# Kernel optimization log

Hardware: AMD Instinct MI355X
Metric: run time of the kernel (lower is better)

## Reference

```python
import jax, jax.numpy as jnp
import numpy as np

B, N, DIM, H, DH = 2, 2048, 512, 8, 64
INNER = H * DH  # == DIM, required by the q.view trick in the original module
STEP = 4


def setup_inputs() -> dict:
    key = jax.random.key(0)
    k1, k2, k3 = jax.random.split(key, 3)
    x = jax.random.normal(k1, (B, N, DIM), jnp.float32)
    # to_qkv: Linear(dim, 4*inner_dim, bias=False); stored as [in, out] for x @ W
    W_qkv = jax.random.normal(k2, (DIM, 4 * INNER), jnp.float32) * 0.02
    # to_out: Linear(2*inner_dim, dim) with bias
    W_out = jax.random.normal(k3, (2 * INNER, DIM), jnp.float32) * 0.02
    b_out = jnp.zeros((DIM,), jnp.float32)
    return {"x": x, "W_qkv": W_qkv, "W_out": W_out, "b_out": b_out}


def reference(x, W_qkv, W_out, b_out):
    b, n, _ = x.shape
    h, dh = H, DH
    scale = dh ** -0.5

    qkvt = x @ W_qkv                       # [b, n, 4*inner]
    q, k, v, t = jnp.split(qkvt, 4, axis=-1)
    to_heads = lambda z: z.reshape(b, n, h, dh).transpose(0, 2, 1, 3)  # [b,h,n,dh]
    q, k, v, t = map(to_heads, (q, k, v, t))

    # pad q by repeating its last row yushu times (note: yushu=4 when n%4==0)
    yushu = STEP - n % STEP
    q = jnp.concatenate([q, jnp.repeat(q[:, :, -1:, :], yushu, axis=2)], axis=2)
    q0 = q.reshape(b, h, STEP, (n + yushu) // STEP, dh)[:, :, 0]  # [b,h,(n+yushu)/4,dh]
    q = jnp.tile(q0, (1, 1, STEP, 1))[:, :, :n]                   # [b,h,n,dh]

    dots = jnp.einsum('bhnd,bhmd->bhnm', q, k) * scale
    attn1 = jax.nn.softmax(dots, axis=-1)

    # fixed distance-decay attention: exp(-|i-j|/e), column-normalized
    pos = jnp.arange(1, n + 1, dtype=x.dtype)
    tg = jnp.abs(pos[None, :] - pos[:, None])                     # [n, n]
    attn2 = jnp.exp(-tg / jnp.exp(jnp.asarray(1.0, x.dtype)))
    # torch: attn2 / attn2.sum(-1) broadcasts [n] over last axis (divides column j by row-sum j)
    attn2 = attn2 / attn2.sum(-1)

    out1 = jnp.einsum('bhnm,bhmd->bhnd', attn1, v)
    out2 = jnp.einsum('nm,bhmd->bhnd', attn2, t)  # attn2 shared across b,h; no repeat needed
    out = jnp.concatenate([out1, out2], axis=-1)   # [b,h,n,2*dh]
    out = out.transpose(0, 2, 1, 3).reshape(b, n, 2 * h * dh)  # b n (h d)
    return out @ W_out + b_out  # dropout=0.0 -> identity
```

## Files before the change

### kernel.cpp

```cpp
#include <hip/hip_runtime.h>

#define NSEQ 2048
#define NB   2
#define NH   8

typedef unsigned short u16;
typedef __attribute__((ext_vector_type(8))) short s8v;
typedef __attribute__((ext_vector_type(4))) float f4v;

static __device__ __forceinline__ u16 f2bf(float f) {
  unsigned u = __float_as_uint(f);
  unsigned r = (u + 0x7fffu + ((u >> 16) & 1u)) >> 16;
  return (u16)r;
}
static __device__ __forceinline__ u16 f2bf_fast(float f) {
  return (u16)((__float_as_uint(f) + 0x8000u) >> 16);
}
static __device__ __forceinline__ unsigned pk2(float a, float b) {
  return (unsigned)f2bf(a) | ((unsigned)f2bf(b) << 16);
}
static __device__ __forceinline__ float bf2f(u16 v) {
  return __uint_as_float(((unsigned)v) << 16);
}

typedef __attribute__((address_space(3))) unsigned int lds_u32;
typedef const __attribute__((address_space(1))) unsigned int glob_u32;
static __device__ __forceinline__ void load16(const void* g, void* l) {
  __builtin_amdgcn_global_load_lds((glob_u32*)g, (lds_u32*)l, 16, 0, 0);
}

__global__ __launch_bounds__(256)
void prep_kernel(const float* __restrict__ x, const float* __restrict__ Wqkv,
                 const float* __restrict__ Wout, u16* __restrict__ xb,
                 u16* __restrict__ WqkvT, u16* __restrict__ Wc) {
  __shared__ float tile[32][33];
  const int bid = blockIdx.x;
  if (bid < 1024) {
    long i = ((long)bid * 256 + threadIdx.x) * 8;
    float4 a = *(const float4*)&x[i];
    float4 b = *(const float4*)&x[i + 4];
    uint4 w;
    w.x = pk2(a.x, a.y); w.y = pk2(a.z, a.w);
    w.z = pk2(b.x, b.y); w.w = pk2(b.z, b.w);
    *(uint4*)&xb[i] = w;
    return;
  }
  const int tx = threadIdx.x & 31, ty = threadIdx.x >> 5;
  if (bid < 2048) {
    int b2 = bid - 1024;
    int c0 = (b2 & 63) * 32, r0 = (b2 >> 6) * 32;
#pragma unroll
    for (int s = 0; s < 32; s += 8)
      tile[ty + s][tx] = Wqkv[(long)(r0 + ty + s) * 2048 + c0 + tx];
    __syncthreads();
#pragma unroll
    for (int s = 0; s < 32; s += 8)
      WqkvT[(long)(c0 + ty + s) * 512 + r0 + tx] = f2bf(tile[tx][ty + s]);
    return;
  }
  {
    int b3 = bid - 2048;
    int part = b3 >= 256;
    if (part) b3 -= 256;
    int c0 = (b3 & 15) * 32, r0 = (b3 >> 4) * 32;
#pragma unroll
    for (int s = 0; s < 32; s += 8) {
      int k = r0 + ty + s;
      int srcrow = ((k >> 6) * 128) + part * 64 + (k & 63);
      tile[ty + s][tx] = Wout[(long)srcrow * 512 + c0 + tx];
    }
    __syncthreads();
    int koff = part ? 0 : 512;
#pragma unroll
    for (int s = 0; s < 32; s += 8) {
      long o = (long)(c0 + ty + s) * 1024 + koff + r0 + tx;
      Wc[o] = f2bf(tile[tx][ty + s]);
    }
  }
}

__global__ __launch_bounds__(256)
void gemm1_fused(const u16* __restrict__ xb, const u16* __restrict__ WqkvT,
                 u16* __restrict__ qkvtb, u16* __restrict__ qu,
                 u16* __restrict__ VtG) {
  const int bid = blockIdx.x;
  const bool isq = bid >= 768;
  int bxk, by;
  if (!isq) { bxk = bid % 24; by = bid / 24; }
  else { int b2 = bid - 768; bxk = b2 & 7; by = b2 >> 3; }
  __shared__ alignas(16) u16 As[128 * 64];
  __shared__ alignas(16) u16 Bs[64 * 64];
  const int tid = threadIdx.x, lane = tid & 63, wave = tid >> 6;
  const int l15 = lane & 15, quad = lane >> 4;
  const int wr = wave >> 1, wc = wave & 1;
  const int Brow0 = isq ? bxk * 64 : 512 + bxk * 64;

  int offA[4], offB[2];
  long baseA[4], baseB[2];
#pragma unroll
  for (int c = 0; c < 4; ++c) {
    int off = (c * 4 + wave) * 1024 + lane * 16;
    int r = off >> 7;
    int cp = (off & 127) >> 4;
    int cb = ((cp ^ (r & 7)) << 3);
    offA[c] = off;
    int gar;
    if (!isq) {
      gar = by * 128 + r;
    } else {
      int rr = by * 128 + r;
      int b = rr >= 576;
      int s = rr - (b ? 576 : 0);
      if (s >= 513) s -= 513;
      gar = b * 2048 + s;
    }
    baseA[c] = (long)gar * 512 + cb;
  }
#pragma unroll
  for (int c = 0; c < 2; ++c) {
    int off = (c * 4 + wave) * 1024 + lane * 16;
    int r = off >> 7, cp = (off & 127) >> 4;
    int cb = ((cp ^ (r & 7)) << 3);
    offB[c] = off;
    baseB[c] = (long)(Brow0 + r) * 512 + cb;
  }

  f4v acc[4][2];
#pragma unroll
  for (int i = 0; i < 4; ++i)
#pragma unroll
    for (int j = 0; j < 2; ++j) acc[i][j] = (f4v){0.f, 0.f, 0.f, 0.f};

  for (int k0 = 0; k0 < 512; k0 += 64) {
    __syncthreads();
#pragma unroll
    for (int c = 0; c < 4; ++c)
      load16(&xb[baseA[c] + k0], ((char*)As) + offA[c]);
#pragma unroll
    for (int c = 0; c < 2; ++c)
      load16(&WqkvT[baseB[c] + k0], ((char*)Bs) + offB[c]);
    __syncthreads();

#pragma unroll
    for (int ksub = 0; ksub < 2; ++ksub) {
      const int cc = (((ksub << 2) | quad) ^ (l15 & 7)) << 3;
      s8v bf[2];
#pragma unroll
      for (int j = 0; j < 2; ++j)
        bf[j] = *(const s8v*)&Bs[(wc * 32 + j * 16 + l15) * 64 + cc];
#pragma unroll
      for (int i = 0; i < 4; ++i) {
        s8v af = *(const s8v*)&As[(wr * 64 + i * 16 + l15) * 64 + cc];
#pragma unroll
        for (int j = 0; j < 2; ++j)
          acc[i][j] = __builtin_amdgcn_mfma_f32_16x16x32_bf16(af, bf[j], acc[i][j], 0, 0, 0);
      }
    }
  }

  const bool isv = (!isq) && bxk >= 8 && bxk < 16;
#pragma unroll
  for (int i = 0; i < 4; ++i) {
    int row0 = by * 128 + wr * 64 + i * 16 + quad * 4;
    if (isv) {
      int b = row0 >> 11, n = row0 & 2047;
#pragma unroll
      for (int j = 0; j < 2; ++j) {
        int vcol = (bxk - 8) * 64 + wc * 32 + j * 16 + l15;
        int h = vcol >> 6, d = vcol & 63;
        uint2 w;
        w.x = pk2(acc[i][j][0], acc[i][j][1]);
        w.y = pk2(acc[i][j][2], acc[i][j][3]);
        *(uint2*)&VtG[(((long)b * 8 + h) * 64 + d) * 2048 + n] = w;
      }
    } else {
#pragma unroll
      for (int rr = 0; rr < 4; ++rr) {
        int row = row0 + rr;
#pragma unroll
        for (int j = 0; j < 2; ++j) {
          int col = wc * 32 + j * 16 + l15;
          u16 v = f2bf(acc[i][j][rr]);
          if (!isq)
            qkvtb[(long)row * 2048 + 512 + bxk * 64 + col] = v;
          else
            qu[(long)row * 512 + bxk * 64 + col] = v;
        }
      }
    }
  }
}

__global__ __launch_bounds__(256)
void gemm2_merged(const u16* __restrict__ O2, const u16* __restrict__ O1u,
                  const u16* __restrict__ Wc, const float* __restrict__ bias,
                  float* __restrict__ C) {
  __shared__ alignas(16) u16 As[64 * 64];
  __shared__ alignas(16) u16 Bs[64 * 64];
  const int tid = threadIdx.x, lane = tid & 63, wave = tid >> 6;
  const int l15 = lane & 15, quad = lane >> 4;
  const int wr = wave >> 1, wc = wave & 1;
  const long m0 = (long)blockIdx.y * 64, n0 = (long)blockIdx.x * 64;

  int offA[2], offB[2];
  long baseO2[2], baseO1[2], baseB[2];
#pragma unroll
  for (int c = 0; c < 2; ++c) {
    int off = (c * 4 + wave) * 1024 + lane * 16;
    int r = off >> 7, cp = (off & 127) >> 4;
    int cb = ((cp ^ (r & 7)) << 3);
    offA[c] = off; offB[c] = off;
    long rowA = m0 + r;
    int b = (int)(rowA >> 11);
    int eff = (int)(rowA & 2047) % 513;
    baseO2[c] = rowA * 512 + cb;
    baseO1[c] = ((long)(b * 576 + eff)) * 512 + cb;
    baseB[c] = (long)(n0 + r) * 1024 + cb;
  }

  f4v acc[2][2];
#pragma unroll
  for (int i = 0; i < 2; ++i)
#pragma unroll
    for (int j = 0; j < 2; ++j) acc[i][j] = (f4v){0.f, 0.f, 0.f, 0.f};

  for (int k0 = 0; k0 < 1024; k0 += 64) {
    __syncthreads();
#pragma unroll
    for (int c = 0; c < 2; ++c) {
      const u16* src = (k0 < 512) ? &O2[baseO2[c] + k0] : &O1u[baseO1[c] + k0 - 512];
      load16(src, ((char*)As) + offA[c]);
      load16(&Wc[baseB[c] + k0], ((char*)Bs) + offB[c]);
    }
    __syncthreads();

#pragma unroll
    for (int ksub = 0; ksub < 2; ++ksub) {
      const int cc = (((ksub << 2) | quad) ^ (l15 & 7)) << 3;
      s8v bf[2];
#pragma unroll
      for (int j = 0; j < 2; ++j)
        bf[j] = *(const s8v*)&Bs[(wc * 32 + j * 16 + l15) * 64 + cc];
#pragma unroll
      for (int i = 0; i < 2; ++i) {
        s8v af = *(const s8v*)&As[(wr * 32 + i * 16 + l15) * 64 + cc];
#pragma unroll
        for (int j = 0; j < 2; ++j)
          acc[i][j] = __builtin_amdgcn_mfma_f32_16x16x32_bf16(af, bf[j], acc[i][j], 0, 0, 0);
      }
    }
  }

#pragma unroll
  for (int i = 0; i < 2; ++i)
#pragma unroll
    for (int rr = 0; rr < 4; ++rr) {
      long row = m0 + wr * 32 + i * 16 + quad * 4 + rr;
#pragma unroll
      for (int j = 0; j < 2; ++j) {
        long col = n0 + wc * 32 + j * 16 + l15;
        C[row * 512 + col] = acc[i][j][rr] + bias[col];
      }
    }
}

struct AttnSm {
  alignas(16) u16 Qs[64 * 64];
  alignas(16) u16 Ks[64 * 64];
  alignas(16) u16 Vt[64 * 64];
  alignas(16) u16 Ps[4][16][72];
};
struct Out2Sm {
  alignas(16) u16 Ts[256 * 64];
  float Is[256];
};

__global__ __launch_bounds__(256)
void attn_out2(const u16* __restrict__ qkvt, const u16* __restrict__ qu,
               const u16* __restrict__ VtG, u16* __restrict__ Opart,
               float* __restrict__ rspart, u16* __restrict__ O2) {
  __shared__ union { AttnSm a; Out2Sm o; } sm;
  const int tid = threadIdx.x;
  const int bid = blockIdx.x;

  if (bid >= 576) {
    const int bid2 = bid - 576;
    const int rg = bid2 & 31;
    const int bh = bid2 >> 5;
    const int b = bh >> 3, h = bh & 7;
    const int g0 = rg * 64 - 96;
#pragma unroll
    for (int c = 0; c < 8; ++c) {
      int chunk = c * 256 + tid;
      int row = chunk >> 3, cc = chunk & 7;
      int gr = g0 + row;
      uint4 w = {0u, 0u, 0u, 0u};
      if (gr >= 0 && gr < NSEQ)
        w = *(const uint4*)&qkvt[((long)(b * NSEQ + gr)) * 2048 + 1536 + h * 64 + cc * 8];
      *(uint4*)&sm.o.Ts[row * 64 + cc * 8] = w;
    }
    {
      const float ie = 0.36787944117144233f;
      const float rr = 0.69220062755534635f;
      const float inv1mr = 1.0f / (1.0f - rr);
      int gr = g0 + tid;
      float val = 0.f;
      if (gr >= 0 && gr < NSEQ) {
        float rj = __expf(-ie * (float)gr);
        float rn = __expf(-ie * (float)(NSEQ - 1 - gr));
        float s = 1.0f + (rr - rr * rj) * inv1mr + (rr - rr * rn) * inv1mr;
        val = 1.0f / s;
      }
      sm.o.Is[tid] = val;
    }
    __syncthreads();

    const int d = tid & 63, sub = tid >> 6;
    const float r = 0.69220062755534635f;
    const int lo = 96 + sub * 16;
    float F = 0.f;
    float Fv[16];
#pragma unroll 8
    for (int j = lo - 96; j < lo; ++j)
      F = F * r + sm.o.Is[j] * bf2f(sm.o.Ts[j * 64 + d]);
#pragma unroll
    for (int k = 0; k < 16; ++k) {
      int j = lo + k;
      F = F * r + sm.o.Is[j] * bf2f(sm.o.Ts[j * 64 + d]);
      Fv[k] = F;
    }
    float G = 0.f;
#pragma unroll 8
    for (int j = lo + 15 + 96; j > lo + 15; --j)
      G = G * r + sm.o.Is[j] * bf2f(sm.o.Ts[j * 64 + d]);
#pragma unroll
    for (int k = 15; k >= 0; --k) {
      int j = lo + k;
      float u = sm.o.Is[j] * bf2f(sm.o.Ts[j * 64 + d]);
      G = G * r + u;
      O2[((long)(b * NSEQ + g0 + j)) * 512 + h * 64 + d] = f2bf(Fv[k] + G - u);
    }
    return;
  }

  const int lane = tid & 63, wave = tid >> 6;
  const int l15  = lane & 15, quad = lane >> 4;
  const int qtile = bid % 9;
  const int t9 = bid / 9;
  const int bh = t9 & 15;
  const int split = t9 >> 4;
  const int b = bh >> 3, h = bh & 7;
  const long rowbase = (long)b * NSEQ;
  const long vtbase = ((long)b * 8 + h) * 64 * 2048;

  int srow[2], scs[2];
#pragma unroll
  for (int p = 0; p < 2; ++p) {
    int idx = p * 256 + tid;
    srow[p] = idx >> 3;
    scs[p] = (idx & 7) ^ (srow[p] & 7);
  }

#pragma unroll
  for (int p = 0; p < 2; ++p) {
    int v = qtile * 64 + srow[p];
    int eff = v >= 513 ? v - 513 : v;
    load16(&qu[((long)(b * 576 + eff)) * 512 + h * 64 + scs[p] * 8],
           (char*)sm.a.Qs + (p * 256 + wave * 64) * 16);
  }
  __syncthreads();

  s8v qf[2];
  {
    const int mrow = wave * 16 + l15;
    const int c0 = quad ^ (mrow & 7);
    qf[0] = *(const s8v*)&sm.a.Qs[mrow * 64 + c0 * 8];
    qf[1] = *(const s8v*)&sm.a.Qs[mrow * 64 + (c0 ^ 4) * 8];
  }

  f4v oacc[4];
#pragma unroll
  for (int i = 0; i < 4; ++i) oacc[i] = (f4v){0.f, 0.f, 0.f, 0.f};
  float rs[4] = {0.f, 0.f, 0.f, 0.f};

  for (int kt = 0; kt < 8; ++kt) {
    __syncthreads();
    const int kb = split * 512 + kt * 64;
#pragma unroll
    for (int p = 0; p < 2; ++p) {
      load16(&qkvt[(rowbase + kb + srow[p]) * 2048 + 512 + h * 64 + scs[p] * 8],
             (char*)sm.a.Ks + (p * 256 + wave * 64) * 16);
      load16(&VtG[vtbase + (long)srow[p] * 2048 + kb + scs[p] * 8],
             (char*)sm.a.Vt + (p * 256 + wave * 64) * 16);
    }
    __syncthreads();

#pragma unroll
    for (int nt = 0; nt < 4; ++nt) {
      f4v s = {0.f, 0.f, 0.f, 0.f};
      const int kr = nt * 16 + l15;
      const int kc0 = quad ^ (kr & 7);
      s8v kf0 = *(const s8v*)&sm.a.Ks[kr * 64 + kc0 * 8];
      s8v kf1 = *(const s8v*)&sm.a.Ks[kr * 64 + (kc0 ^ 4) * 8];
      s = __builtin_amdgcn_mfma_f32_16x16x32_bf16(qf[0], kf0, s, 0, 0, 0);
      s = __builtin_amdgcn_mfma_f32_16x16x32_bf16(qf[1], kf1, s, 0, 0, 0);
#pragma unroll
      for (int rr = 0; rr < 4; ++rr) {
        float p = __expf(s[rr] * 0.125f);
        rs[rr] += p;
        sm.a.Ps[wave][quad * 4 + rr][nt * 16 + l15] = f2bf_fast(p);
      }
    }
    asm volatile("" ::: "memory");

    s8v pf0 = *(const s8v*)&sm.a.Ps[wave][l15][quad * 8];
    s8v pf1 = *(const s8v*)&sm.a.Ps[wave][l15][32 + quad * 8];
#pragma unroll
    for (int nt = 0; nt < 4; ++nt) {
      const int vr = nt * 16 + l15;
      const int vc0 = quad ^ (vr & 7);
      s8v vf0 = *(const s8v*)&sm.a.Vt[vr * 64 + vc0 * 8];
      s8v vf1 = *(const s8v*)&sm.a.Vt[vr * 64 + (vc0 ^ 4) * 8];
      oacc[nt] = __builtin_amdgcn_mfma_f32_16x16x32_bf16(pf0, vf0, oacc[nt], 0, 0, 0);
      oacc[nt] = __builtin_amdgcn_mfma_f32_16x16x32_bf16(pf1, vf1, oacc[nt], 0, 0, 0);
    }
  }

  const long sb = ((long)split * 16 + bh) * 576;
#pragma unroll
  for (int rr = 0; rr < 4; ++rr) {
    float t = rs[rr];
    t += __shfl_xor(t, 1);
    t += __shfl_xor(t, 2);
    t += __shfl_xor(t, 4);
    t += __shfl_xor(t, 8);
    int row = qtile * 64 + wave * 16 + quad * 4 + rr;
    if (l15 == 0) rspart[sb + row] = t;
#pragma unroll
    for (int nt = 0; nt < 4; ++nt)
      Opart[(sb + row) * 64 + nt * 16 + l15] = f2bf(oacc[nt][rr]);
  }
}

__global__ __launch_bounds__(256)
void attn_combine(const u16* __restrict__ Opart, const float* __restrict__ rspart,
                  u16* __restrict__ O1u) {
  int idx = blockIdx.x * 256 + threadIdx.x;
  int d4 = idx & 15, rowbh = idx >> 4;
  int bh = rowbh / 576, row = rowbh - bh * 576;
  int b = bh >> 3, h = bh & 7;
  float o[4] = {0.f, 0.f, 0.f, 0.f};
  float rsum = 0.f;
#pragma unroll
  for (int s = 0; s < 4; ++s) {
    long base = ((long)s * 16 + bh) * 576 + row;
    const u16* p = &Opart[base * 64 + d4 * 4];
    uint2 v = *(const uint2*)p;
    o[0] += bf2f((u16)(v.x & 0xffff));
    o[1] += bf2f((u16)(v.x >> 16));
    o[2] += bf2f((u16)(v.y & 0xffff));
    o[3] += bf2f((u16)(v.y >> 16));
    rsum += rspart[base];
  }
  float inv = 1.0f / rsum;
  uint2 w = {pk2(o[0] * inv, o[1] * inv), pk2(o[2] * inv, o[3] * inv)};
  *(uint2*)&O1u[((long)(b * 576 + row)) * 512 + h * 64 + d4 * 4] = w;
}

extern "C" void kernel_launch(void* const* d_in, const int* in_sizes, int n_in,
                              void* d_out, int out_size, void* d_ws, size_t ws_size,
                              hipStream_t stream) {
  (void)in_sizes; (void)n_in; (void)out_size; (void)ws_size;
  const float* x    = (const float*)d_in[0];
  const float* Wqkv = (const float*)d_in[1];
  const float* Wout = (const float*)d_in[2];
  const float* bout = (const float*)d_in[3];
  float* out = (float*)d_out;

  u16*   qkvtb = (u16*)d_ws;
  u16*   qu    = qkvtb + (size_t)4096 * 2048;
  u16*   VtG   = qu    + (size_t)1152 * 512;
  u16*   O2    = VtG   + (size_t)2 * 8 * 64 * 2048;
  u16*   O1u   = O2    + (size_t)4096 * 512;
  u16*   xb    = O1u   + (size_t)1152 * 512;
  u16*   WqkvT = xb    + (size_t)4096 * 512;
  u16*   Wc    = WqkvT + (size_t)2048 * 512;
  u16*   Opart = Wc    + (size_t)512 * 1024;
  float* rsp   = (float*)(Opart + (size_t)4 * 16 * 576 * 64);

  prep_kernel<<<dim3(2560), 256, 0, stream>>>(x, Wqkv, Wout, xb, WqkvT, Wc);
  gemm1_fused<<<dim3(840), 256, 0, stream>>>(xb, WqkvT, qkvtb, qu, VtG);
  attn_out2<<<dim3(1088), 256, 0, stream>>>(qkvtb, qu, VtG, Opart, rsp, O2);
  attn_combine<<<dim3(576), 256, 0, stream>>>(Opart, rsp, O1u);
  gemm2_merged<<<dim3(8, 64), 256, 0, stream>>>(O2, O1u, Wc, bout, out);
}
```

Baseline: 119.2 us.

## Drop split-K attention and combine kernel; normalize output in attention kernel

Removes the 4-way split over the key dimension in the attention kernel, so each block now loops over all 32 key tiles and normalizes its output directly. This eliminates the separate combine kernel launch and the partial-output and row-sum buffers in global memory. The trade-off is fewer attention blocks (144 instead of 576), which lowers parallelism and leaves each block with a serial chain four times longer.

```diff
diff --git a/kernel.cpp b/kernel.cpp
--- a/kernel.cpp
+++ b/kernel.cpp
@@ -277,14 +277,14 @@
 
 __global__ __launch_bounds__(256)
 void attn_out2(const u16* __restrict__ qkvt, const u16* __restrict__ qu,
-               const u16* __restrict__ VtG, u16* __restrict__ Opart,
-               float* __restrict__ rspart, u16* __restrict__ O2) {
+               const u16* __restrict__ VtG, u16* __restrict__ O1u,
+               u16* __restrict__ O2) {
   __shared__ union { AttnSm a; Out2Sm o; } sm;
   const int tid = threadIdx.x;
   const int bid = blockIdx.x;
 
-  if (bid >= 576) {
-    const int bid2 = bid - 576;
+  if (bid >= 144) {
+    const int bid2 = bid - 144;
     const int rg = bid2 & 31;
     const int bh = bid2 >> 5;
     const int b = bh >> 3, h = bh & 7;
@@ -346,9 +346,7 @@
   const int lane = tid & 63, wave = tid >> 6;
   const int l15  = lane & 15, quad = lane >> 4;
   const int qtile = bid % 9;
-  const int t9 = bid / 9;
-  const int bh = t9 & 15;
-  const int split = t9 >> 4;
+  const int bh = bid / 9;
   const int b = bh >> 3, h = bh & 7;
   const long rowbase = (long)b * NSEQ;
   const long vtbase = ((long)b * 8 + h) * 64 * 2048;
@@ -383,9 +381,9 @@
   for (int i = 0; i < 4; ++i) oacc[i] = (f4v){0.f, 0.f, 0.f, 0.f};
   float rs[4] = {0.f, 0.f, 0.f, 0.f};
 
-  for (int kt = 0; kt < 8; ++kt) {
-    __syncthreads();
-    const int kb = split * 512 + kt * 64;
+  for (int kt = 0; kt < 32; ++kt) {
+    __syncthreads();
+    const int kb = kt * 64;
 #pragma unroll
     for (int p = 0; p < 2; ++p) {
       load16(&qkvt[(rowbase + kb + srow[p]) * 2048 + 512 + h * 64 + scs[p] * 8],
@@ -426,7 +424,6 @@
     }
   }
 
-  const long sb = ((long)split * 16 + bh) * 576;
 #pragma unroll
   for (int rr = 0; rr < 4; ++rr) {
     float t = rs[rr];
@@ -434,37 +431,13 @@
     t += __shfl_xor(t, 2);
     t += __shfl_xor(t, 4);
     t += __shfl_xor(t, 8);
+    float inv = 1.0f / t;
     int row = qtile * 64 + wave * 16 + quad * 4 + rr;
-    if (l15 == 0) rspart[sb + row] = t;
 #pragma unroll
     for (int nt = 0; nt < 4; ++nt)
-      Opart[(sb + row) * 64 + nt * 16 + l15] = f2bf(oacc[nt][rr]);
-  }
-}
-
-__global__ __launch_bounds__(256)
-void attn_combine(const u16* __restrict__ Opart, const float* __restrict__ rspart,
-                  u16* __restrict__ O1u) {
-  int idx = blockIdx.x * 256 + threadIdx.x;
-  int d4 = idx & 15, rowbh = idx >> 4;
-  int bh = rowbh / 576, row = rowbh - bh * 576;
-  int b = bh >> 3, h = bh & 7;
-  float o[4] = {0.f, 0.f, 0.f, 0.f};
-  float rsum = 0.f;
-#pragma unroll
-  for (int s = 0; s < 4; ++s) {
-    long base = ((long)s * 16 + bh) * 576 + row;
-    const u16* p = &Opart[base * 64 + d4 * 4];
-    uint2 v = *(const uint2*)p;
-    o[0] += bf2f((u16)(v.x & 0xffff));
-    o[1] += bf2f((u16)(v.x >> 16));
-    o[2] += bf2f((u16)(v.y & 0xffff));
-    o[3] += bf2f((u16)(v.y >> 16));
-    rsum += rspart[base];
-  }
-  float inv = 1.0f / rsum;
-  uint2 w = {pk2(o[0] * inv, o[1] * inv), pk2(o[2] * inv, o[3] * inv)};
-  *(uint2*)&O1u[((long)(b * 576 + row)) * 512 + h * 64 + d4 * 4] = w;
+      O1u[((long)(b * 576 + row)) * 512 + h * 64 + nt * 16 + l15] =
+          f2bf(oacc[nt][rr] * inv);
+  }
 }
 
 extern "C" void kernel_launch(void* const* d_in, const int* in_sizes, int n_in,
@@ -485,12 +458,9 @@
   u16*   xb    = O1u   + (size_t)1152 * 512;
   u16*   WqkvT = xb    + (size_t)4096 * 512;
   u16*   Wc    = WqkvT + (size_t)2048 * 512;
-  u16*   Opart = Wc    + (size_t)512 * 1024;
-  float* rsp   = (float*)(Opart + (size_t)4 * 16 * 576 * 64);
 
   prep_kernel<<<dim3(2560), 256, 0, stream>>>(x, Wqkv, Wout, xb, WqkvT, Wc);
   gemm1_fused<<<dim3(840), 256, 0, stream>>>(xb, WqkvT, qkvtb, qu, VtG);
-  attn_out2<<<dim3(1088), 256, 0, stream>>>(qkvtb, qu, VtG, Opart, rsp, O2);
-  attn_combine<<<dim3(576), 256, 0, stream>>>(Opart, rsp, O1u);
+  attn_out2<<<dim3(656), 256, 0, stream>>>(qkvtb, qu, VtG, O1u, O2);
   gemm2_merged<<<dim3(8, 64), 256, 0, stream>>>(O2, O1u, Wc, bout, out);
 }
```

Measured after the change: 132.2 us. 1.11x slower.
